# Kernel optimization log

Hardware: AMD Instinct MI355X
Metric: run time of the kernel (lower is better)

Reference implementation:

```python
import jax, jax.numpy as jnp
import numpy as np

N_SRC = 100000
N_DST = 100000
E = 500000
D = 128      # in_units
F = 64       # efeat_dim
NB = 2       # num_basis
C = 5        # num_classes


def setup_inputs() -> dict:
    key = jax.random.key(0)
    ks = jax.random.split(key, 14)
    s = 1.0 / np.sqrt(D)
    return {
        "h_src": jax.random.normal(ks[0], (N_SRC, D), jnp.float32),
        "h_dst": jax.random.normal(ks[1], (N_DST, D), jnp.float32),
        "efeats": jax.random.normal(ks[2], (E, F), jnp.float32),
        "u_idx": jax.random.randint(ks[3], (E,), 0, N_SRC),
        "v_idx": jax.random.randint(ks[4], (E,), 0, N_DST),
        "W1": jax.random.normal(ks[5], (D, F), jnp.float32) * (1.0 / np.sqrt(F)),
        "b1": jnp.zeros((D,), jnp.float32),
        "W2": jax.random.normal(ks[6], (D, D), jnp.float32) * s,
        "b2": jnp.zeros((D,), jnp.float32),
        "W3": jax.random.normal(ks[7], (D, D), jnp.float32) * s,
        "b3": jnp.zeros((D,), jnp.float32),
        "W_comb": jax.random.normal(ks[8], (D, 2 * D), jnp.float32) * (1.0 / np.sqrt(2 * D)),
        "P": jax.random.normal(ks[9], (NB, D, D), jnp.float32) * s,
        "W_cb": jax.random.normal(ks[10], (C, NB), jnp.float32) * (1.0 / np.sqrt(NB)),
    }


def reference(h_src, h_dst, efeats, u_idx, v_idx,
              W1, b1, W2, b2, W3, b3, W_comb, P, W_cb):
    # 3-layer edge-feature MLP (dropout is identity at eval / rate=0)
    e = jax.nn.relu(efeats @ W1.T + b1)   # [E, D]
    e = jax.nn.relu(e @ W2.T + b2)        # [E, D]
    e = e @ W3.T + b3                     # [E, D]
    # gather node feats by edge endpoints, concat with transformed efeats, combine
    u = jnp.concatenate([h_src[u_idx], e], axis=1) @ W_comb.T  # [E, D]
    v = jnp.concatenate([h_dst[v_idx], e], axis=1) @ W_comb.T  # [E, D]
    # bilinear basis decode: out[e, b] = u[e] @ P[b] @ v[e]
    out = jnp.einsum('ei,bij,ej->eb', u, P, v)  # [E, NB]
    return out @ W_cb.T                          # [E, C]
```

## Files before the change

### kernel.cpp

```cpp
#include <hip/hip_runtime.h>
#include <hip/hip_bf16.h>

#define NNODE 100000
#define EDG   500000
#define DD    128
#define FF    64
#define NCLS  5

#define OFF_W1   0
#define OFF_W2   8192
#define OFF_W3   24576
#define OFF_WCR  40960
#define OFF_WCL  57344
#define OFF_P0   73728
#define OFF_P1   90112
#define OFF_HU   106496
#define OFF_HV   (106496 + NNODE * DD)
#define PREP_TOT 106496

typedef __attribute__((ext_vector_type(8))) short short8;
typedef __attribute__((ext_vector_type(4))) float f32x4;

union U4 { uint4 v; ushort s[8]; };

__device__ __forceinline__ float bf2f(ushort u) {
  return __uint_as_float(((unsigned int)u) << 16);
}
__device__ __forceinline__ ushort f2bf(float f) {
  unsigned int u = __float_as_uint(f);
  u += 0x7FFF + ((u >> 16) & 1);
  return (ushort)(u >> 16);
}
__device__ __forceinline__ ushort2 pk2(float a, float b) {
  __hip_bfloat162 t = __float22bfloat162_rn(make_float2(a, b));
  return *(ushort2*)&t;
}
__device__ __forceinline__ ushort4 pk4(float a, float b, float c, float d) {
  ushort2 lo = pk2(a, b), hi = pk2(c, d);
  ushort4 o; o.x = lo.x; o.y = lo.y; o.z = hi.x; o.w = hi.y; return o;
}

__device__ __forceinline__ int sw(int row, int col) {
  return row * 128 + ((((col >> 3) ^ (row & 7)) << 3) | (col & 7));
}

__device__ __forceinline__ void zacc(f32x4 a[2][4]) {
#pragma unroll
  for (int i = 0; i < 2; ++i)
#pragma unroll
    for (int j = 0; j < 4; ++j)
      a[i][j] = (f32x4){0.f, 0.f, 0.f, 0.f};
}

__device__ __forceinline__ void gemm_T(const ushort* act,
                                       const ushort* __restrict__ W, int K,
                                       int ksteps, f32x4 acc[2][4],
                                       int m0, int l15, int q) {
  for (int ks = 0; ks < ksteps; ++ks) {
    const int ko = ks * 32 + q * 8;
    short8 a0 = *(const short8*)(W + (m0 + l15) * K + ko);
    short8 a1 = *(const short8*)(W + (m0 + 16 + l15) * K + ko);
#pragma unroll
    for (int nt = 0; nt < 4; ++nt) {
      short8 b = *(const short8*)&act[sw(nt * 16 + l15, ko)];
      acc[0][nt] = __builtin_amdgcn_mfma_f32_16x16x32_bf16(a0, b, acc[0][nt], 0, 0, 0);
      acc[1][nt] = __builtin_amdgcn_mfma_f32_16x16x32_bf16(a1, b, acc[1][nt], 0, 0, 0);
    }
  }
}

__device__ __forceinline__ void store_T(ushort* dst, f32x4 acc[2][4],
                                        const float* __restrict__ bias, int relu,
                                        int m0, int l15, int q) {
#pragma unroll
  for (int mt = 0; mt < 2; ++mt) {
    const int feat = m0 + mt * 16 + q * 4;
    float4 bv = bias ? *(const float4*)(bias + feat) : make_float4(0.f, 0.f, 0.f, 0.f);
#pragma unroll
    for (int nt = 0; nt < 4; ++nt) {
      const int edge = nt * 16 + l15;
      float v0 = acc[mt][nt][0] + bv.x, v1 = acc[mt][nt][1] + bv.y;
      float v2 = acc[mt][nt][2] + bv.z, v3 = acc[mt][nt][3] + bv.w;
      if (relu) {
        v0 = fmaxf(v0, 0.f); v1 = fmaxf(v1, 0.f);
        v2 = fmaxf(v2, 0.f); v3 = fmaxf(v3, 0.f);
      }
      *(ushort4*)&dst[sw(edge, feat)] = pk4(v0, v1, v2, v3);
    }
  }
}

__global__ void __launch_bounds__(256) prep_kernel(
    const float* __restrict__ W1, const float* __restrict__ W2,
    const float* __restrict__ W3, const float* __restrict__ W_comb,
    const float* __restrict__ P, ushort* __restrict__ ws) {
  int idx = blockIdx.x * 256 + threadIdx.x;
  if (idx >= PREP_TOT) return;
  float val;
  if (idx < 8192) {
    val = W1[idx];
  } else {
    int r = idx - 8192, m = r >> 14, rr = r & 16383;
    switch (m) {
      case 0:  val = W2[rr]; break;
      case 1:  val = W3[rr]; break;
      case 2:  { int n = rr >> 7, k = rr & 127; val = W_comb[n * 256 + 128 + k]; } break;
      case 3:  { int n = rr >> 7, k = rr & 127; val = W_comb[n * 256 + k]; } break;
      case 4:  val = P[rr]; break;
      default: val = P[16384 + rr]; break;
    }
  }
  ws[idx] = f2bf(val);
}

__global__ void __launch_bounds__(256, 4) node_kernel(
    const float* __restrict__ h_src, const float* __restrict__ h_dst,
    ushort* __restrict__ ws) {
  __shared__ ushort BUF[2][64][128];
  ushort* A = &BUF[0][0][0];
  ushort* B = &BUF[1][0][0];
  const int NT = (NNODE + 63) / 64;
  const int tid = threadIdx.x;
  const int w = tid >> 6, lane = tid & 63, l15 = lane & 15, q = lane >> 4;
  const int m0 = w * 32;
  const int bb = blockIdx.x;
  const float* h = (bb < NT) ? h_src : h_dst;
  ushort* op = ws + ((bb < NT) ? OFF_HU : OFF_HV);
  const int r0 = ((bb < NT) ? bb : bb - NT) * 64;
  const int srow = tid >> 2, part = tid & 3;
  int row = r0 + srow; if (row >= NNODE) row = NNODE - 1;
  {
    const float4* src = (const float4*)(h + (long)row * DD) + part * 8;
#pragma unroll
    for (int c = 0; c < 4; ++c) {
      float4 v0 = src[c * 2], v1 = src[c * 2 + 1];
      U4 o;
      *(ushort4*)&o.s[0] = pk4(v0.x, v0.y, v0.z, v0.w);
      *(ushort4*)&o.s[4] = pk4(v1.x, v1.y, v1.z, v1.w);
      *(uint4*)&A[sw(srow, part * 32 + c * 8)] = o.v;
    }
  }
  __syncthreads();
  f32x4 acc[2][4];
  zacc(acc);
  gemm_T(A, ws + OFF_WCL, 128, 4, acc, m0, l15, q);
  store_T(B, acc, nullptr, 0, m0, l15, q);
  __syncthreads();
  if (r0 + srow < NNODE) {
    uint4* d = (uint4*)(op + (long)(r0 + srow) * DD + part * 32);
#pragma unroll
    for (int i = 0; i < 4; ++i)
      d[i] = *(const uint4*)&B[sw(srow, part * 32 + i * 8)];
  }
}

__global__ void __launch_bounds__(256, 4) edge_kernel(
    const float* __restrict__ efeats, const int* __restrict__ u_idx,
    const int* __restrict__ v_idx, const float* __restrict__ b1,
    const float* __restrict__ b2, const float* __restrict__ b3,
    const float* __restrict__ W_cb, const ushort* __restrict__ ws,
    float* __restrict__ out) {
  __shared__ ushort BUF[2][64][128];
  __shared__ float OB[64][2];
  ushort* A = &BUF[0][0][0];
  ushort* B = &BUF[1][0][0];

  const int tid = threadIdx.x;
  const int lane = tid & 63;
  const int l15 = lane & 15, q = lane >> 4;
  const int m0 = (tid >> 6) * 32;
  const long e0 = (long)blockIdx.x * 64;

  const int srow = tid >> 2, part = tid & 3;
  long grow = e0 + srow; if (grow >= EDG) grow = EDG - 1;
  const int vi = v_idx[grow], ui = u_idx[grow];

  {
    const float4* src = (const float4*)(efeats + grow * FF) + part * 4;
#pragma unroll
    for (int c = 0; c < 2; ++c) {
      float4 v0 = src[c * 2], v1 = src[c * 2 + 1];
      U4 o;
      *(ushort4*)&o.s[0] = pk4(v0.x, v0.y, v0.z, v0.w);
      *(ushort4*)&o.s[4] = pk4(v1.x, v1.y, v1.z, v1.w);
      *(uint4*)&A[sw(srow, part * 16 + c * 8)] = o.v;
    }
  }
  __syncthreads();

  f32x4 acc[2][4];
  zacc(acc); gemm_T(A, ws + OFF_W1, 64, 2, acc, m0, l15, q);
  store_T(B, acc, b1, 1, m0, l15, q);
  __syncthreads();
  zacc(acc); gemm_T(B, ws + OFF_W2, 128, 4, acc, m0, l15, q);
  store_T(A, acc, b2, 1, m0, l15, q);
  __syncthreads();
  zacc(acc); gemm_T(A, ws + OFF_W3, 128, 4, acc, m0, l15, q);
  store_T(B, acc, b3, 0, m0, l15, q);
  __syncthreads();

  uint4 hvp[4];
  {
    const uint4* hp = (const uint4*)(ws + OFF_HV + (long)vi * DD + part * 32);
#pragma unroll
    for (int c = 0; c < 4; ++c) hvp[c] = hp[c];
  }
  zacc(acc); gemm_T(B, ws + OFF_WCR, 128, 4, acc, m0, l15, q);
  store_T(A, acc, nullptr, 0, m0, l15, q);
  __syncthreads();

  {
#pragma unroll
    for (int c = 0; c < 4; ++c) {
      U4 a; a.v = hvp[c];
      U4 e; e.v = *(const uint4*)&A[sw(srow, part * 32 + c * 8)];
      U4 o;
#pragma unroll
      for (int j = 0; j < 8; j += 2) {
        ushort2 p = pk2(bf2f(a.s[j]) + bf2f(e.s[j]),
                        bf2f(a.s[j + 1]) + bf2f(e.s[j + 1]));
        o.s[j] = p.x; o.s[j + 1] = p.y;
      }
      *(uint4*)&B[sw(srow, part * 32 + c * 8)] = o.v;
    }
    if (tid < 128) OB[tid >> 1][tid & 1] = 0.f;
  }
  __syncthreads();

  uint4 hup[4];
  {
    const uint4* hp = (const uint4*)(ws + OFF_HU + (long)ui * DD + part * 32);
#pragma unroll
    for (int c = 0; c < 4; ++c) hup[c] = hp[c];
  }

  f32x4 tacc[2][2][4];
  zacc(tacc[0]); zacc(tacc[1]);
  for (int ks = 0; ks < 4; ++ks) {
    const int ko = ks * 32 + q * 8;
    short8 a00 = *(const short8*)(ws + OFF_P0 + (m0 + l15) * 128 + ko);
    short8 a01 = *(const short8*)(ws + OFF_P0 + (m0 + 16 + l15) * 128 + ko);
    short8 a10 = *(const short8*)(ws + OFF_P1 + (m0 + l15) * 128 + ko);
    short8 a11 = *(const short8*)(ws + OFF_P1 + (m0 + 16 + l15) * 128 + ko);
#pragma unroll
    for (int nt = 0; nt < 4; ++nt) {
      short8 b = *(const short8*)&B[sw(nt * 16 + l15, ko)];
      tacc[0][0][nt] = __builtin_amdgcn_mfma_f32_16x16x32_bf16(a00, b, tacc[0][0][nt], 0, 0, 0);
      tacc[0][1][nt] = __builtin_amdgcn_mfma_f32_16x16x32_bf16(a01, b, tacc[0][1][nt], 0, 0, 0);
      tacc[1][0][nt] = __builtin_amdgcn_mfma_f32_16x16x32_bf16(a10, b, tacc[1][0][nt], 0, 0, 0);
      tacc[1][1][nt] = __builtin_amdgcn_mfma_f32_16x16x32_bf16(a11, b, tacc[1][1][nt], 0, 0, 0);
    }
  }
  __syncthreads();

  {
#pragma unroll
    for (int c = 0; c < 4; ++c) {
      U4 a; a.v = hup[c];
      U4 e; e.v = *(const uint4*)&A[sw(srow, part * 32 + c * 8)];
      U4 o;
#pragma unroll
      for (int j = 0; j < 8; j += 2) {
        ushort2 p = pk2(bf2f(a.s[j]) + bf2f(e.s[j]),
                        bf2f(a.s[j + 1]) + bf2f(e.s[j + 1]));
        o.s[j] = p.x; o.s[j + 1] = p.y;
      }
      *(uint4*)&B[sw(srow, part * 32 + c * 8)] = o.v;
    }
  }
  __syncthreads();

#pragma unroll
  for (int nt = 0; nt < 4; ++nt) {
    const int edge = nt * 16 + l15;
    float pb0 = 0.f, pb1 = 0.f;
#pragma unroll
    for (int mt = 0; mt < 2; ++mt) {
      ushort4 u4 = *(const ushort4*)&B[sw(edge, m0 + mt * 16 + q * 4)];
      float uf;
      uf = bf2f(u4.x); pb0 += tacc[0][mt][nt][0] * uf; pb1 += tacc[1][mt][nt][0] * uf;
      uf = bf2f(u4.y); pb0 += tacc[0][mt][nt][1] * uf; pb1 += tacc[1][mt][nt][1] * uf;
      uf = bf2f(u4.z); pb0 += tacc[0][mt][nt][2] * uf; pb1 += tacc[1][mt][nt][2] * uf;
      uf = bf2f(u4.w); pb0 += tacc[0][mt][nt][3] * uf; pb1 += tacc[1][mt][nt][3] * uf;
    }
    pb0 += __shfl_xor(pb0, 16, 64); pb0 += __shfl_xor(pb0, 32, 64);
    pb1 += __shfl_xor(pb1, 16, 64); pb1 += __shfl_xor(pb1, 32, 64);
    if (q == 0) {
      atomicAdd(&OB[edge][0], pb0);
      atomicAdd(&OB[edge][1], pb1);
    }
  }
  __syncthreads();

  for (int t = tid; t < 64 * NCLS; t += 256) {
    int r = t / NCLS, c = t % NCLS;
    long erow = e0 + r;
    if (erow < EDG) {
      out[erow * NCLS + c] = OB[r][0] * W_cb[c * 2] + OB[r][1] * W_cb[c * 2 + 1];
    }
  }
}

extern "C" void kernel_launch(void* const* d_in, const int* in_sizes, int n_in,
                              void* d_out, int out_size, void* d_ws,
                              size_t ws_size, hipStream_t stream) {
  const float* h_src  = (const float*)d_in[0];
  const float* h_dst  = (const float*)d_in[1];
  const float* efeats = (const float*)d_in[2];
  const int*   u_idx  = (const int*)d_in[3];
  const int*   v_idx  = (const int*)d_in[4];
  const float* W1     = (const float*)d_in[5];
  const float* b1     = (const float*)d_in[6];
  const float* W2     = (const float*)d_in[7];
  const float* b2     = (const float*)d_in[8];
  const float* W3     = (const float*)d_in[9];
  const float* b3     = (const float*)d_in[10];
  const float* W_comb = (const float*)d_in[11];
  const float* P      = (const float*)d_in[12];
  const float* W_cb   = (const float*)d_in[13];
  ushort* ws = (ushort*)d_ws;
  float* out = (float*)d_out;

  prep_kernel<<<(PREP_TOT + 255) / 256, 256, 0, stream>>>(W1, W2, W3, W_comb, P, ws);
  node_kernel<<<2 * ((NNODE + 63) / 64), 256, 0, stream>>>(h_src, h_dst, ws);
  edge_kernel<<<(EDG + 63) / 64, 256, 0, stream>>>(efeats, u_idx, v_idx,
                                                   b1, b2, b3, W_cb, ws, out);
}
```

Measured before the change: 461.4 us.

## Make node and edge kernels persistent with register-resident weights and input prefetch

Both node_kernel and edge_kernel become persistent grids of 1024 blocks that loop over 64-row tiles. Each block loads the W_comb-left, W1, W2 and W3 MFMA fragments into registers once, and prefetches the next tile's inputs (features and u/v indices) while the current tile computes. The edge kernel also gathers h_u and h_v together and builds both combined vectors in one pass, which removes one barrier. In exchange, register use goes up: edge launch bounds drop to 2 blocks per CU, which lowers occupancy.

```diff
diff --git a/kernel.cpp b/kernel.cpp
--- a/kernel.cpp
+++ b/kernel.cpp
@@ -18,6 +18,9 @@
 #define OFF_HV   (106496 + NNODE * DD)
 #define PREP_TOT 106496
 
+#define NODE_GRID 1024
+#define EDGE_GRID 1024
+
 typedef __attribute__((ext_vector_type(8))) short short8;
 typedef __attribute__((ext_vector_type(4))) float f32x4;
 
@@ -50,6 +53,21 @@
 #pragma unroll
     for (int j = 0; j < 4; ++j)
       a[i][j] = (f32x4){0.f, 0.f, 0.f, 0.f};
+}
+
+template <int KS>
+__device__ __forceinline__ void gemm_R(const ushort* act, const short8 af[][2],
+                                       f32x4 acc[2][4], int l15, int q) {
+#pragma unroll
+  for (int ks = 0; ks < KS; ++ks) {
+    const int ko = ks * 32 + q * 8;
+#pragma unroll
+    for (int nt = 0; nt < 4; ++nt) {
+      short8 b = *(const short8*)&act[sw(nt * 16 + l15, ko)];
+      acc[0][nt] = __builtin_amdgcn_mfma_f32_16x16x32_bf16(af[ks][0], b, acc[0][nt], 0, 0, 0);
+      acc[1][nt] = __builtin_amdgcn_mfma_f32_16x16x32_bf16(af[ks][1], b, acc[1][nt], 0, 0, 0);
+    }
+  }
 }
 
 __device__ __forceinline__ void gemm_T(const ushort* act,
@@ -120,41 +138,73 @@
   ushort* A = &BUF[0][0][0];
   ushort* B = &BUF[1][0][0];
   const int NT = (NNODE + 63) / 64;
+  const int TIL = 2 * NT;
   const int tid = threadIdx.x;
-  const int w = tid >> 6, lane = tid & 63, l15 = lane & 15, q = lane >> 4;
-  const int m0 = w * 32;
-  const int bb = blockIdx.x;
-  const float* h = (bb < NT) ? h_src : h_dst;
-  ushort* op = ws + ((bb < NT) ? OFF_HU : OFF_HV);
-  const int r0 = ((bb < NT) ? bb : bb - NT) * 64;
+  const int lane = tid & 63, l15 = lane & 15, q = lane >> 4;
+  const int m0 = (tid >> 6) * 32;
   const int srow = tid >> 2, part = tid & 3;
-  int row = r0 + srow; if (row >= NNODE) row = NNODE - 1;
+
+  short8 aW[4][2];
   {
-    const float4* src = (const float4*)(h + (long)row * DD) + part * 8;
+    const ushort* Wp = ws + OFF_WCL;
+#pragma unroll
+    for (int ks = 0; ks < 4; ++ks) {
+      const int ko = ks * 32 + q * 8;
+      aW[ks][0] = *(const short8*)(Wp + (m0 + l15) * 128 + ko);
+      aW[ks][1] = *(const short8*)(Wp + (m0 + 16 + l15) * 128 + ko);
+    }
+  }
+  float4 xr[8];
+  {
+    const int t0 = blockIdx.x;
+    const float* h = (t0 < NT) ? h_src : h_dst;
+    int r = ((t0 < NT) ? t0 : t0 - NT) * 64 + srow;
+    if (r >= NNODE) r = NNODE - 1;
+    const float4* src = (const float4*)(h + (long)r * DD) + part * 8;
+#pragma unroll
+    for (int c = 0; c < 8; ++c) xr[c] = src[c];
+  }
+
+  for (int t = blockIdx.x; t < TIL; t += NODE_GRID) {
 #pragma unroll
     for (int c = 0; c < 4; ++c) {
-      float4 v0 = src[c * 2], v1 = src[c * 2 + 1];
+      float4 v0 = xr[c * 2], v1 = xr[c * 2 + 1];
       U4 o;
       *(ushort4*)&o.s[0] = pk4(v0.x, v0.y, v0.z, v0.w);
       *(ushort4*)&o.s[4] = pk4(v1.x, v1.y, v1.z, v1.w);
       *(uint4*)&A[sw(srow, part * 32 + c * 8)] = o.v;
     }
-  }
-  __syncthreads();
-  f32x4 acc[2][4];
-  zacc(acc);
-  gemm_T(A, ws + OFF_WCL, 128, 4, acc, m0, l15, q);
-  store_T(B, acc, nullptr, 0, m0, l15, q);
-  __syncthreads();
-  if (r0 + srow < NNODE) {
-    uint4* d = (uint4*)(op + (long)(r0 + srow) * DD + part * 32);
-#pragma unroll
-    for (int i = 0; i < 4; ++i)
-      d[i] = *(const uint4*)&B[sw(srow, part * 32 + i * 8)];
-  }
-}
-
-__global__ void __launch_bounds__(256, 4) edge_kernel(
+    __syncthreads();
+    {
+      int tn = t + NODE_GRID;
+      if (tn < TIL) {
+        const float* h = (tn < NT) ? h_src : h_dst;
+        int r = ((tn < NT) ? tn : tn - NT) * 64 + srow;
+        if (r >= NNODE) r = NNODE - 1;
+        const float4* src = (const float4*)(h + (long)r * DD) + part * 8;
+#pragma unroll
+        for (int c = 0; c < 8; ++c) xr[c] = src[c];
+      }
+    }
+    f32x4 acc[2][4];
+    zacc(acc);
+    gemm_R<4>(A, aW, acc, l15, q);
+    store_T(B, acc, nullptr, 0, m0, l15, q);
+    __syncthreads();
+    {
+      const int r0 = ((t < NT) ? t : t - NT) * 64;
+      ushort* op = ws + ((t < NT) ? OFF_HU : OFF_HV);
+      if (r0 + srow < NNODE) {
+        uint4* d = (uint4*)(op + (long)(r0 + srow) * DD + part * 32);
+#pragma unroll
+        for (int i = 0; i < 4; ++i)
+          d[i] = *(const uint4*)&B[sw(srow, part * 32 + i * 8)];
+      }
+    }
+  }
+}
+
+__global__ void __launch_bounds__(256, 2) edge_kernel(
     const float* __restrict__ efeats, const int* __restrict__ u_idx,
     const int* __restrict__ v_idx, const float* __restrict__ b1,
     const float* __restrict__ b2, const float* __restrict__ b3,
@@ -169,135 +219,148 @@
   const int lane = tid & 63;
   const int l15 = lane & 15, q = lane >> 4;
   const int m0 = (tid >> 6) * 32;
-  const long e0 = (long)blockIdx.x * 64;
-
   const int srow = tid >> 2, part = tid & 3;
-  long grow = e0 + srow; if (grow >= EDG) grow = EDG - 1;
-  const int vi = v_idx[grow], ui = u_idx[grow];
-
+  const int TIL = (EDG + 63) / 64;
+
+  short8 a1f[2][2], a2f[4][2], a3f[4][2];
+#pragma unroll
+  for (int ks = 0; ks < 2; ++ks) {
+    const int ko = ks * 32 + q * 8;
+    a1f[ks][0] = *(const short8*)(ws + OFF_W1 + (m0 + l15) * 64 + ko);
+    a1f[ks][1] = *(const short8*)(ws + OFF_W1 + (m0 + 16 + l15) * 64 + ko);
+  }
+#pragma unroll
+  for (int ks = 0; ks < 4; ++ks) {
+    const int ko = ks * 32 + q * 8;
+    a2f[ks][0] = *(const short8*)(ws + OFF_W2 + (m0 + l15) * 128 + ko);
+    a2f[ks][1] = *(const short8*)(ws + OFF_W2 + (m0 + 16 + l15) * 128 + ko);
+    a3f[ks][0] = *(const short8*)(ws + OFF_W3 + (m0 + l15) * 128 + ko);
+    a3f[ks][1] = *(const short8*)(ws + OFF_W3 + (m0 + 16 + l15) * 128 + ko);
+  }
+  float wcb[2 * NCLS];
+#pragma unroll
+  for (int i = 0; i < 2 * NCLS; ++i) wcb[i] = W_cb[i];
+
+  float4 xr[4];
+  int ui, vi;
   {
-    const float4* src = (const float4*)(efeats + grow * FF) + part * 4;
+    long g = (long)blockIdx.x * 64 + srow;
+    if (g >= EDG) g = EDG - 1;
+    ui = u_idx[g]; vi = v_idx[g];
+    const float4* src = (const float4*)(efeats + g * FF) + part * 4;
+#pragma unroll
+    for (int c = 0; c < 4; ++c) xr[c] = src[c];
+  }
+
+  for (long t = blockIdx.x; t < TIL; t += EDGE_GRID) {
+    const long e0 = t * 64;
 #pragma unroll
     for (int c = 0; c < 2; ++c) {
-      float4 v0 = src[c * 2], v1 = src[c * 2 + 1];
+      float4 v0 = xr[c * 2], v1 = xr[c * 2 + 1];
       U4 o;
       *(ushort4*)&o.s[0] = pk4(v0.x, v0.y, v0.z, v0.w);
       *(ushort4*)&o.s[4] = pk4(v1.x, v1.y, v1.z, v1.w);
       *(uint4*)&A[sw(srow, part * 16 + c * 8)] = o.v;
     }
-  }
-  __syncthreads();
-
-  f32x4 acc[2][4];
-  zacc(acc); gemm_T(A, ws + OFF_W1, 64, 2, acc, m0, l15, q);
-  store_T(B, acc, b1, 1, m0, l15, q);
-  __syncthreads();
-  zacc(acc); gemm_T(B, ws + OFF_W2, 128, 4, acc, m0, l15, q);
-  store_T(A, acc, b2, 1, m0, l15, q);
-  __syncthreads();
-  zacc(acc); gemm_T(A, ws + OFF_W3, 128, 4, acc, m0, l15, q);
-  store_T(B, acc, b3, 0, m0, l15, q);
-  __syncthreads();
-
-  uint4 hvp[4];
-  {
-    const uint4* hp = (const uint4*)(ws + OFF_HV + (long)vi * DD + part * 32);
-#pragma unroll
-    for (int c = 0; c < 4; ++c) hvp[c] = hp[c];
-  }
-  zacc(acc); gemm_T(B, ws + OFF_WCR, 128, 4, acc, m0, l15, q);
-  store_T(A, acc, nullptr, 0, m0, l15, q);
-  __syncthreads();
-
-  {
+    __syncthreads();
+    int un = ui, vn = vi;
+    {
+      long tn = t + EDGE_GRID;
+      if (tn < TIL) {
+        long g = tn * 64 + srow;
+        if (g >= EDG) g = EDG - 1;
+        un = u_idx[g]; vn = v_idx[g];
+        const float4* src = (const float4*)(efeats + g * FF) + part * 4;
+#pragma unroll
+        for (int c = 0; c < 4; ++c) xr[c] = src[c];
+      }
+    }
+    f32x4 acc[2][4];
+    zacc(acc); gemm_R<2>(A, a1f, acc, l15, q);
+    store_T(B, acc, b1, 1, m0, l15, q);
+    __syncthreads();
+    zacc(acc); gemm_R<4>(B, a2f, acc, l15, q);
+    store_T(A, acc, b2, 1, m0, l15, q);
+    __syncthreads();
+    uint4 hvp[4], hup[4];
+    {
+      const uint4* hv = (const uint4*)(ws + OFF_HV + (long)vi * DD + part * 32);
+      const uint4* hu = (const uint4*)(ws + OFF_HU + (long)ui * DD + part * 32);
+#pragma unroll
+      for (int c = 0; c < 4; ++c) hvp[c] = hv[c];
+#pragma unroll
+      for (int c = 0; c < 4; ++c) hup[c] = hu[c];
+    }
+    zacc(acc); gemm_R<4>(A, a3f, acc, l15, q);
+    store_T(B, acc, b3, 0, m0, l15, q);
+    __syncthreads();
+    zacc(acc); gemm_T(B, ws + OFF_WCR, 128, 4, acc, m0, l15, q);
+    store_T(A, acc, nullptr, 0, m0, l15, q);
+    __syncthreads();
 #pragma unroll
     for (int c = 0; c < 4; ++c) {
-      U4 a; a.v = hvp[c];
       U4 e; e.v = *(const uint4*)&A[sw(srow, part * 32 + c * 8)];
-      U4 o;
+      U4 hv_; hv_.v = hvp[c];
+      U4 hu_; hu_.v = hup[c];
+      U4 vo, uo;
 #pragma unroll
       for (int j = 0; j < 8; j += 2) {
-        ushort2 p = pk2(bf2f(a.s[j]) + bf2f(e.s[j]),
-                        bf2f(a.s[j + 1]) + bf2f(e.s[j + 1]));
-        o.s[j] = p.x; o.s[j + 1] = p.y;
-      }
-      *(uint4*)&B[sw(srow, part * 32 + c * 8)] = o.v;
+        float ea = bf2f(e.s[j]), eb = bf2f(e.s[j + 1]);
+        ushort2 pv = pk2(bf2f(hv_.s[j]) + ea, bf2f(hv_.s[j + 1]) + eb);
+        ushort2 pu = pk2(bf2f(hu_.s[j]) + ea, bf2f(hu_.s[j + 1]) + eb);
+        vo.s[j] = pv.x; vo.s[j + 1] = pv.y;
+        uo.s[j] = pu.x; uo.s[j + 1] = pu.y;
+      }
+      *(uint4*)&B[sw(srow, part * 32 + c * 8)] = vo.v;
+      *(uint4*)&A[sw(srow, part * 32 + c * 8)] = uo.v;
     }
     if (tid < 128) OB[tid >> 1][tid & 1] = 0.f;
-  }
-  __syncthreads();
-
-  uint4 hup[4];
-  {
-    const uint4* hp = (const uint4*)(ws + OFF_HU + (long)ui * DD + part * 32);
-#pragma unroll
-    for (int c = 0; c < 4; ++c) hup[c] = hp[c];
-  }
-
-  f32x4 tacc[2][2][4];
-  zacc(tacc[0]); zacc(tacc[1]);
-  for (int ks = 0; ks < 4; ++ks) {
-    const int ko = ks * 32 + q * 8;
-    short8 a00 = *(const short8*)(ws + OFF_P0 + (m0 + l15) * 128 + ko);
-    short8 a01 = *(const short8*)(ws + OFF_P0 + (m0 + 16 + l15) * 128 + ko);
-    short8 a10 = *(const short8*)(ws + OFF_P1 + (m0 + l15) * 128 + ko);
-    short8 a11 = *(const short8*)(ws + OFF_P1 + (m0 + 16 + l15) * 128 + ko);
+    __syncthreads();
+    f32x4 tacc[2][2][4];
+    zacc(tacc[0]); zacc(tacc[1]);
+    for (int ks = 0; ks < 4; ++ks) {
+      const int ko = ks * 32 + q * 8;
+      short8 a00 = *(const short8*)(ws + OFF_P0 + (m0 + l15) * 128 + ko);
+      short8 a01 = *(const short8*)(ws + OFF_P0 + (m0 + 16 + l15) * 128 + ko);
+      short8 a10 = *(const short8*)(ws + OFF_P1 + (m0 + l15) * 128 + ko);
+      short8 a11 = *(const short8*)(ws + OFF_P1 + (m0 + 16 + l15) * 128 + ko);
+#pragma unroll
+      for (int nt = 0; nt < 4; ++nt) {
+        short8 b = *(const short8*)&B[sw(nt * 16 + l15, ko)];
+        tacc[0][0][nt] = __builtin_amdgcn_mfma_f32_16x16x32_bf16(a00, b, tacc[0][0][nt], 0, 0, 0);
+        tacc[0][1][nt] = __builtin_amdgcn_mfma_f32_16x16x32_bf16(a01, b, tacc[0][1][nt], 0, 0, 0);
+        tacc[1][0][nt] = __builtin_amdgcn_mfma_f32_16x16x32_bf16(a10, b, tacc[1][0][nt], 0, 0, 0);
+        tacc[1][1][nt] = __builtin_amdgcn_mfma_f32_16x16x32_bf16(a11, b, tacc[1][1][nt], 0, 0, 0);
+      }
+    }
 #pragma unroll
     for (int nt = 0; nt < 4; ++nt) {
-      short8 b = *(const short8*)&B[sw(nt * 16 + l15, ko)];
-      tacc[0][0][nt] = __builtin_amdgcn_mfma_f32_16x16x32_bf16(a00, b, tacc[0][0][nt], 0, 0, 0);
-      tacc[0][1][nt] = __builtin_amdgcn_mfma_f32_16x16x32_bf16(a01, b, tacc[0][1][nt], 0, 0, 0);
-      tacc[1][0][nt] = __builtin_amdgcn_mfma_f32_16x16x32_bf16(a10, b, tacc[1][0][nt], 0, 0, 0);
-      tacc[1][1][nt] = __builtin_amdgcn_mfma_f32_16x16x32_bf16(a11, b, tacc[1][1][nt], 0, 0, 0);
-    }
-  }
-  __syncthreads();
-
-  {
-#pragma unroll
-    for (int c = 0; c < 4; ++c) {
-      U4 a; a.v = hup[c];
-      U4 e; e.v = *(const uint4*)&A[sw(srow, part * 32 + c * 8)];
-      U4 o;
-#pragma unroll
-      for (int j = 0; j < 8; j += 2) {
-        ushort2 p = pk2(bf2f(a.s[j]) + bf2f(e.s[j]),
-                        bf2f(a.s[j + 1]) + bf2f(e.s[j + 1]));
-        o.s[j] = p.x; o.s[j + 1] = p.y;
-      }
-      *(uint4*)&B[sw(srow, part * 32 + c * 8)] = o.v;
-    }
-  }
-  __syncthreads();
-
-#pragma unroll
-  for (int nt = 0; nt < 4; ++nt) {
-    const int edge = nt * 16 + l15;
-    float pb0 = 0.f, pb1 = 0.f;
-#pragma unroll
-    for (int mt = 0; mt < 2; ++mt) {
-      ushort4 u4 = *(const ushort4*)&B[sw(edge, m0 + mt * 16 + q * 4)];
-      float uf;
-      uf = bf2f(u4.x); pb0 += tacc[0][mt][nt][0] * uf; pb1 += tacc[1][mt][nt][0] * uf;
-      uf = bf2f(u4.y); pb0 += tacc[0][mt][nt][1] * uf; pb1 += tacc[1][mt][nt][1] * uf;
-      uf = bf2f(u4.z); pb0 += tacc[0][mt][nt][2] * uf; pb1 += tacc[1][mt][nt][2] * uf;
-      uf = bf2f(u4.w); pb0 += tacc[0][mt][nt][3] * uf; pb1 += tacc[1][mt][nt][3] * uf;
-    }
-    pb0 += __shfl_xor(pb0, 16, 64); pb0 += __shfl_xor(pb0, 32, 64);
-    pb1 += __shfl_xor(pb1, 16, 64); pb1 += __shfl_xor(pb1, 32, 64);
-    if (q == 0) {
-      atomicAdd(&OB[edge][0], pb0);
-      atomicAdd(&OB[edge][1], pb1);
-    }
-  }
-  __syncthreads();
-
-  for (int t = tid; t < 64 * NCLS; t += 256) {
-    int r = t / NCLS, c = t % NCLS;
-    long erow = e0 + r;
-    if (erow < EDG) {
-      out[erow * NCLS + c] = OB[r][0] * W_cb[c * 2] + OB[r][1] * W_cb[c * 2 + 1];
-    }
+      const int edge = nt * 16 + l15;
+      float pb0 = 0.f, pb1 = 0.f;
+#pragma unroll
+      for (int mt = 0; mt < 2; ++mt) {
+        ushort4 u4 = *(const ushort4*)&A[sw(edge, m0 + mt * 16 + q * 4)];
+        float uf;
+        uf = bf2f(u4.x); pb0 += tacc[0][mt][nt][0] * uf; pb1 += tacc[1][mt][nt][0] * uf;
+        uf = bf2f(u4.y); pb0 += tacc[0][mt][nt][1] * uf; pb1 += tacc[1][mt][nt][1] * uf;
+        uf = bf2f(u4.z); pb0 += tacc[0][mt][nt][2] * uf; pb1 += tacc[1][mt][nt][2] * uf;
+        uf = bf2f(u4.w); pb0 += tacc[0][mt][nt][3] * uf; pb1 += tacc[1][mt][nt][3] * uf;
+      }
+      pb0 += __shfl_xor(pb0, 16, 64); pb0 += __shfl_xor(pb0, 32, 64);
+      pb1 += __shfl_xor(pb1, 16, 64); pb1 += __shfl_xor(pb1, 32, 64);
+      if (q == 0) {
+        atomicAdd(&OB[edge][0], pb0);
+        atomicAdd(&OB[edge][1], pb1);
+      }
+    }
+    __syncthreads();
+    for (int tt = tid; tt < 64 * NCLS; tt += 256) {
+      int r = tt / NCLS, c = tt % NCLS;
+      long erow = e0 + r;
+      if (erow < EDG)
+        out[erow * NCLS + c] = OB[r][0] * wcb[c * 2] + OB[r][1] * wcb[c * 2 + 1];
+    }
+    ui = un; vi = vn;
   }
 }
 
@@ -322,7 +385,7 @@
   float* out = (float*)d_out;
 
   prep_kernel<<<(PREP_TOT + 255) / 256, 256, 0, stream>>>(W1, W2, W3, W_comb, P, ws);
-  node_kernel<<<2 * ((NNODE + 63) / 64), 256, 0, stream>>>(h_src, h_dst, ws);
-  edge_kernel<<<(EDG + 63) / 64, 256, 0, stream>>>(efeats, u_idx, v_idx,
-                                                   b1, b2, b3, W_cb, ws, out);
-}
+  node_kernel<<<NODE_GRID, 256, 0, stream>>>(h_src, h_dst, ws);
+  edge_kernel<<<EDGE_GRID, 256, 0, stream>>>(efeats, u_idx, v_idx,
+                                             b1, b2, b3, W_cb, ws, out);
+}
```

New measurement: 578.3 us. 25.3% more time.

## Double threads per block to 512, each wave owning 16 output features

Applied to the files above, without the earlier changes.

Node and edge kernels now launch 512 threads (8 waves) per 64-row tile instead of 256, with each wave computing a 16-feature slice rather than 32. Loads, gathers, elementwise combines and the bilinear reduction are re-partitioned so each thread handles half as much data. The aim is more waves in flight to hide gather and global-load latency, and fewer registers per thread. In exchange, weight-fragment loads are spread across more waves, barriers cover more waves, and more shared-memory atomics contend on the output buffer.

```diff
diff --git a/kernel.cpp b/kernel.cpp
--- a/kernel.cpp
+++ b/kernel.cpp
@@ -44,49 +44,42 @@
   return row * 128 + ((((col >> 3) ^ (row & 7)) << 3) | (col & 7));
 }
 
-__device__ __forceinline__ void zacc(f32x4 a[2][4]) {
-#pragma unroll
-  for (int i = 0; i < 2; ++i)
-#pragma unroll
-    for (int j = 0; j < 4; ++j)
-      a[i][j] = (f32x4){0.f, 0.f, 0.f, 0.f};
-}
-
-__device__ __forceinline__ void gemm_T(const ushort* act,
-                                       const ushort* __restrict__ W, int K,
-                                       int ksteps, f32x4 acc[2][4],
-                                       int m0, int l15, int q) {
+
+__device__ __forceinline__ void zacc1(f32x4 a[4]) {
+#pragma unroll
+  for (int j = 0; j < 4; ++j) a[j] = (f32x4){0.f, 0.f, 0.f, 0.f};
+}
+
+__device__ __forceinline__ void gemm_T1(const ushort* act,
+                                        const ushort* __restrict__ W, int K,
+                                        int ksteps, f32x4 acc[4],
+                                        int m0, int l15, int q) {
   for (int ks = 0; ks < ksteps; ++ks) {
     const int ko = ks * 32 + q * 8;
     short8 a0 = *(const short8*)(W + (m0 + l15) * K + ko);
-    short8 a1 = *(const short8*)(W + (m0 + 16 + l15) * K + ko);
 #pragma unroll
     for (int nt = 0; nt < 4; ++nt) {
       short8 b = *(const short8*)&act[sw(nt * 16 + l15, ko)];
-      acc[0][nt] = __builtin_amdgcn_mfma_f32_16x16x32_bf16(a0, b, acc[0][nt], 0, 0, 0);
-      acc[1][nt] = __builtin_amdgcn_mfma_f32_16x16x32_bf16(a1, b, acc[1][nt], 0, 0, 0);
-    }
-  }
-}
-
-__device__ __forceinline__ void store_T(ushort* dst, f32x4 acc[2][4],
-                                        const float* __restrict__ bias, int relu,
-                                        int m0, int l15, int q) {
-#pragma unroll
-  for (int mt = 0; mt < 2; ++mt) {
-    const int feat = m0 + mt * 16 + q * 4;
-    float4 bv = bias ? *(const float4*)(bias + feat) : make_float4(0.f, 0.f, 0.f, 0.f);
-#pragma unroll
-    for (int nt = 0; nt < 4; ++nt) {
-      const int edge = nt * 16 + l15;
-      float v0 = acc[mt][nt][0] + bv.x, v1 = acc[mt][nt][1] + bv.y;
-      float v2 = acc[mt][nt][2] + bv.z, v3 = acc[mt][nt][3] + bv.w;
-      if (relu) {
-        v0 = fmaxf(v0, 0.f); v1 = fmaxf(v1, 0.f);
-        v2 = fmaxf(v2, 0.f); v3 = fmaxf(v3, 0.f);
-      }
-      *(ushort4*)&dst[sw(edge, feat)] = pk4(v0, v1, v2, v3);
-    }
+      acc[nt] = __builtin_amdgcn_mfma_f32_16x16x32_bf16(a0, b, acc[nt], 0, 0, 0);
+    }
+  }
+}
+
+__device__ __forceinline__ void store_T1(ushort* dst, f32x4 acc[4],
+                                         const float* __restrict__ bias, int relu,
+                                         int m0, int l15, int q) {
+  const int feat = m0 + q * 4;
+  float4 bv = bias ? *(const float4*)(bias + feat) : make_float4(0.f, 0.f, 0.f, 0.f);
+#pragma unroll
+  for (int nt = 0; nt < 4; ++nt) {
+    const int edge = nt * 16 + l15;
+    float v0 = acc[nt][0] + bv.x, v1 = acc[nt][1] + bv.y;
+    float v2 = acc[nt][2] + bv.z, v3 = acc[nt][3] + bv.w;
+    if (relu) {
+      v0 = fmaxf(v0, 0.f); v1 = fmaxf(v1, 0.f);
+      v2 = fmaxf(v2, 0.f); v3 = fmaxf(v3, 0.f);
+    }
+    *(ushort4*)&dst[sw(edge, feat)] = pk4(v0, v1, v2, v3);
   }
 }
 
@@ -113,7 +106,7 @@
   ws[idx] = f2bf(val);
 }
 
-__global__ void __launch_bounds__(256, 4) node_kernel(
+__global__ void __launch_bounds__(512, 6) node_kernel(
     const float* __restrict__ h_src, const float* __restrict__ h_dst,
     ushort* __restrict__ ws) {
   __shared__ ushort BUF[2][64][128];
@@ -121,40 +114,40 @@
   ushort* B = &BUF[1][0][0];
   const int NT = (NNODE + 63) / 64;
   const int tid = threadIdx.x;
-  const int w = tid >> 6, lane = tid & 63, l15 = lane & 15, q = lane >> 4;
-  const int m0 = w * 32;
+  const int lane = tid & 63, l15 = lane & 15, q = lane >> 4;
+  const int m0 = (tid >> 6) * 16;
   const int bb = blockIdx.x;
   const float* h = (bb < NT) ? h_src : h_dst;
   ushort* op = ws + ((bb < NT) ? OFF_HU : OFF_HV);
   const int r0 = ((bb < NT) ? bb : bb - NT) * 64;
-  const int srow = tid >> 2, part = tid & 3;
+  const int srow = tid >> 3, part = tid & 7;
   int row = r0 + srow; if (row >= NNODE) row = NNODE - 1;
   {
-    const float4* src = (const float4*)(h + (long)row * DD) + part * 8;
-#pragma unroll
-    for (int c = 0; c < 4; ++c) {
+    const float4* src = (const float4*)(h + (long)row * DD) + part * 4;
+#pragma unroll
+    for (int c = 0; c < 2; ++c) {
       float4 v0 = src[c * 2], v1 = src[c * 2 + 1];
       U4 o;
       *(ushort4*)&o.s[0] = pk4(v0.x, v0.y, v0.z, v0.w);
       *(ushort4*)&o.s[4] = pk4(v1.x, v1.y, v1.z, v1.w);
-      *(uint4*)&A[sw(srow, part * 32 + c * 8)] = o.v;
-    }
-  }
-  __syncthreads();
-  f32x4 acc[2][4];
-  zacc(acc);
-  gemm_T(A, ws + OFF_WCL, 128, 4, acc, m0, l15, q);
-  store_T(B, acc, nullptr, 0, m0, l15, q);
+      *(uint4*)&A[sw(srow, part * 16 + c * 8)] = o.v;
+    }
+  }
+  __syncthreads();
+  f32x4 acc[4];
+  zacc1(acc);
+  gemm_T1(A, ws + OFF_WCL, 128, 4, acc, m0, l15, q);
+  store_T1(B, acc, nullptr, 0, m0, l15, q);
   __syncthreads();
   if (r0 + srow < NNODE) {
-    uint4* d = (uint4*)(op + (long)(r0 + srow) * DD + part * 32);
-#pragma unroll
-    for (int i = 0; i < 4; ++i)
-      d[i] = *(const uint4*)&B[sw(srow, part * 32 + i * 8)];
-  }
-}
-
-__global__ void __launch_bounds__(256, 4) edge_kernel(
+    uint4* d = (uint4*)(op + (long)(r0 + srow) * DD + part * 16);
+#pragma unroll
+    for (int i = 0; i < 2; ++i)
+      d[i] = *(const uint4*)&B[sw(srow, part * 16 + i * 8)];
+  }
+}
+
+__global__ void __launch_bounds__(512, 6) edge_kernel(
     const float* __restrict__ efeats, const int* __restrict__ u_idx,
     const int* __restrict__ v_idx, const float* __restrict__ b1,
     const float* __restrict__ b2, const float* __restrict__ b3,
@@ -168,52 +161,48 @@
   const int tid = threadIdx.x;
   const int lane = tid & 63;
   const int l15 = lane & 15, q = lane >> 4;
-  const int m0 = (tid >> 6) * 32;
+  const int m0 = (tid >> 6) * 16;
   const long e0 = (long)blockIdx.x * 64;
 
-  const int srow = tid >> 2, part = tid & 3;
+  const int srow = tid >> 3, part = tid & 7;
   long grow = e0 + srow; if (grow >= EDG) grow = EDG - 1;
   const int vi = v_idx[grow], ui = u_idx[grow];
 
   {
-    const float4* src = (const float4*)(efeats + grow * FF) + part * 4;
+    const float4* src = (const float4*)(efeats + grow * FF) + part * 2;
+    float4 v0 = src[0], v1 = src[1];
+    U4 o;
+    *(ushort4*)&o.s[0] = pk4(v0.x, v0.y, v0.z, v0.w);
+    *(ushort4*)&o.s[4] = pk4(v1.x, v1.y, v1.z, v1.w);
+    *(uint4*)&A[sw(srow, part * 8)] = o.v;
+  }
+  __syncthreads();
+
+  f32x4 acc[4];
+  zacc1(acc); gemm_T1(A, ws + OFF_W1, 64, 2, acc, m0, l15, q);
+  store_T1(B, acc, b1, 1, m0, l15, q);
+  __syncthreads();
+  zacc1(acc); gemm_T1(B, ws + OFF_W2, 128, 4, acc, m0, l15, q);
+  store_T1(A, acc, b2, 1, m0, l15, q);
+  __syncthreads();
+  zacc1(acc); gemm_T1(A, ws + OFF_W3, 128, 4, acc, m0, l15, q);
+  store_T1(B, acc, b3, 0, m0, l15, q);
+  __syncthreads();
+
+  uint4 hvp[2];
+  {
+    const uint4* hp = (const uint4*)(ws + OFF_HV + (long)vi * DD) + part * 2;
+    hvp[0] = hp[0]; hvp[1] = hp[1];
+  }
+  zacc1(acc); gemm_T1(B, ws + OFF_WCR, 128, 4, acc, m0, l15, q);
+  store_T1(A, acc, nullptr, 0, m0, l15, q);
+  __syncthreads();
+
+  {
 #pragma unroll
     for (int c = 0; c < 2; ++c) {
-      float4 v0 = src[c * 2], v1 = src[c * 2 + 1];
-      U4 o;
-      *(ushort4*)&o.s[0] = pk4(v0.x, v0.y, v0.z, v0.w);
-      *(ushort4*)&o.s[4] = pk4(v1.x, v1.y, v1.z, v1.w);
-      *(uint4*)&A[sw(srow, part * 16 + c * 8)] = o.v;
-    }
-  }
-  __syncthreads();
-
-  f32x4 acc[2][4];
-  zacc(acc); gemm_T(A, ws + OFF_W1, 64, 2, acc, m0, l15, q);
-  store_T(B, acc, b1, 1, m0, l15, q);
-  __syncthreads();
-  zacc(acc); gemm_T(B, ws + OFF_W2, 128, 4, acc, m0, l15, q);
-  store_T(A, acc, b2, 1, m0, l15, q);
-  __syncthreads();
-  zacc(acc); gemm_T(A, ws + OFF_W3, 128, 4, acc, m0, l15, q);
-  store_T(B, acc, b3, 0, m0, l15, q);
-  __syncthreads();
-
-  uint4 hvp[4];
-  {
-    const uint4* hp = (const uint4*)(ws + OFF_HV + (long)vi * DD + part * 32);
-#pragma unroll
-    for (int c = 0; c < 4; ++c) hvp[c] = hp[c];
-  }
-  zacc(acc); gemm_T(B, ws + OFF_WCR, 128, 4, acc, m0, l15, q);
-  store_T(A, acc, nullptr, 0, m0, l15, q);
-  __syncthreads();
-
-  {
-#pragma unroll
-    for (int c = 0; c < 4; ++c) {
       U4 a; a.v = hvp[c];
-      U4 e; e.v = *(const uint4*)&A[sw(srow, part * 32 + c * 8)];
+      U4 e; e.v = *(const uint4*)&A[sw(srow, part * 16 + c * 8)];
       U4 o;
 #pragma unroll
       for (int j = 0; j < 8; j += 2) {
@@ -221,43 +210,38 @@
                         bf2f(a.s[j + 1]) + bf2f(e.s[j + 1]));
         o.s[j] = p.x; o.s[j + 1] = p.y;
       }
-      *(uint4*)&B[sw(srow, part * 32 + c * 8)] = o.v;
+      *(uint4*)&B[sw(srow, part * 16 + c * 8)] = o.v;
     }
     if (tid < 128) OB[tid >> 1][tid & 1] = 0.f;
   }
   __syncthreads();
 
-  uint4 hup[4];
-  {
-    const uint4* hp = (const uint4*)(ws + OFF_HU + (long)ui * DD + part * 32);
-#pragma unroll
-    for (int c = 0; c < 4; ++c) hup[c] = hp[c];
-  }
-
-  f32x4 tacc[2][2][4];
-  zacc(tacc[0]); zacc(tacc[1]);
+  uint4 hup[2];
+  {
+    const uint4* hp = (const uint4*)(ws + OFF_HU + (long)ui * DD) + part * 2;
+    hup[0] = hp[0]; hup[1] = hp[1];
+  }
+
+  f32x4 tacc[2][4];
+  zacc1(tacc[0]); zacc1(tacc[1]);
   for (int ks = 0; ks < 4; ++ks) {
     const int ko = ks * 32 + q * 8;
-    short8 a00 = *(const short8*)(ws + OFF_P0 + (m0 + l15) * 128 + ko);
-    short8 a01 = *(const short8*)(ws + OFF_P0 + (m0 + 16 + l15) * 128 + ko);
-    short8 a10 = *(const short8*)(ws + OFF_P1 + (m0 + l15) * 128 + ko);
-    short8 a11 = *(const short8*)(ws + OFF_P1 + (m0 + 16 + l15) * 128 + ko);
+    short8 a0 = *(const short8*)(ws + OFF_P0 + (m0 + l15) * 128 + ko);
+    short8 a1 = *(const short8*)(ws + OFF_P1 + (m0 + l15) * 128 + ko);
 #pragma unroll
     for (int nt = 0; nt < 4; ++nt) {
       short8 b = *(const short8*)&B[sw(nt * 16 + l15, ko)];
-      tacc[0][0][nt] = __builtin_amdgcn_mfma_f32_16x16x32_bf16(a00, b, tacc[0][0][nt], 0, 0, 0);
-      tacc[0][1][nt] = __builtin_amdgcn_mfma_f32_16x16x32_bf16(a01, b, tacc[0][1][nt], 0, 0, 0);
-      tacc[1][0][nt] = __builtin_amdgcn_mfma_f32_16x16x32_bf16(a10, b, tacc[1][0][nt], 0, 0, 0);
-      tacc[1][1][nt] = __builtin_amdgcn_mfma_f32_16x16x32_bf16(a11, b, tacc[1][1][nt], 0, 0, 0);
-    }
-  }
-  __syncthreads();
-
-  {
-#pragma unroll
-    for (int c = 0; c < 4; ++c) {
+      tacc[0][nt] = __builtin_amdgcn_mfma_f32_16x16x32_bf16(a0, b, tacc[0][nt], 0, 0, 0);
+      tacc[1][nt] = __builtin_amdgcn_mfma_f32_16x16x32_bf16(a1, b, tacc[1][nt], 0, 0, 0);
+    }
+  }
+  __syncthreads();
+
+  {
+#pragma unroll
+    for (int c = 0; c < 2; ++c) {
       U4 a; a.v = hup[c];
-      U4 e; e.v = *(const uint4*)&A[sw(srow, part * 32 + c * 8)];
+      U4 e; e.v = *(const uint4*)&A[sw(srow, part * 16 + c * 8)];
       U4 o;
 #pragma unroll
       for (int j = 0; j < 8; j += 2) {
@@ -265,7 +249,7 @@
                         bf2f(a.s[j + 1]) + bf2f(e.s[j + 1]));
         o.s[j] = p.x; o.s[j + 1] = p.y;
       }
-      *(uint4*)&B[sw(srow, part * 32 + c * 8)] = o.v;
+      *(uint4*)&B[sw(srow, part * 16 + c * 8)] = o.v;
     }
   }
   __syncthreads();
@@ -274,15 +258,12 @@
   for (int nt = 0; nt < 4; ++nt) {
     const int edge = nt * 16 + l15;
     float pb0 = 0.f, pb1 = 0.f;
-#pragma unroll
-    for (int mt = 0; mt < 2; ++mt) {
-      ushort4 u4 = *(const ushort4*)&B[sw(edge, m0 + mt * 16 + q * 4)];
-      float uf;
-      uf = bf2f(u4.x); pb0 += tacc[0][mt][nt][0] * uf; pb1 += tacc[1][mt][nt][0] * uf;
-      uf = bf2f(u4.y); pb0 += tacc[0][mt][nt][1] * uf; pb1 += tacc[1][mt][nt][1] * uf;
-      uf = bf2f(u4.z); pb0 += tacc[0][mt][nt][2] * uf; pb1 += tacc[1][mt][nt][2] * uf;
-      uf = bf2f(u4.w); pb0 += tacc[0][mt][nt][3] * uf; pb1 += tacc[1][mt][nt][3] * uf;
-    }
+    ushort4 u4 = *(const ushort4*)&B[sw(edge, m0 + q * 4)];
+    float uf;
+    uf = bf2f(u4.x); pb0 += tacc[0][nt][0] * uf; pb1 += tacc[1][nt][0] * uf;
+    uf = bf2f(u4.y); pb0 += tacc[0][nt][1] * uf; pb1 += tacc[1][nt][1] * uf;
+    uf = bf2f(u4.z); pb0 += tacc[0][nt][2] * uf; pb1 += tacc[1][nt][2] * uf;
+    uf = bf2f(u4.w); pb0 += tacc[0][nt][3] * uf; pb1 += tacc[1][nt][3] * uf;
     pb0 += __shfl_xor(pb0, 16, 64); pb0 += __shfl_xor(pb0, 32, 64);
     pb1 += __shfl_xor(pb1, 16, 64); pb1 += __shfl_xor(pb1, 32, 64);
     if (q == 0) {
@@ -292,8 +273,8 @@
   }
   __syncthreads();
 
-  for (int t = tid; t < 64 * NCLS; t += 256) {
-    int r = t / NCLS, c = t % NCLS;
+  if (tid < 64 * NCLS) {
+    int r = tid / NCLS, c = tid % NCLS;
     long erow = e0 + r;
     if (erow < EDG) {
       out[erow * NCLS + c] = OB[r][0] * W_cb[c * 2] + OB[r][1] * W_cb[c * 2 + 1];
@@ -322,7 +303,7 @@
   float* out = (float*)d_out;
 
   prep_kernel<<<(PREP_TOT + 255) / 256, 256, 0, stream>>>(W1, W2, W3, W_comb, P, ws);
-  node_kernel<<<2 * ((NNODE + 63) / 64), 256, 0, stream>>>(h_src, h_dst, ws);
-  edge_kernel<<<(EDG + 63) / 64, 256, 0, stream>>>(efeats, u_idx, v_idx,
+  node_kernel<<<2 * ((NNODE + 63) / 64), 512, 0, stream>>>(h_src, h_dst, ws);
+  edge_kernel<<<(EDG + 63) / 64, 512, 0, stream>>>(efeats, u_idx, v_idx,
                                                    b1, b2, b3, W_cb, ws, out);
 }
```

Result: slower. 472.7 us (+2.5%).
